# Kernel optimization log

Hardware: AMD Instinct MI355X
Metric: run time of the kernel (lower is better)

## Reference

```python
import jax, jax.numpy as jnp
import numpy as np

# Fixed supermask = [3, 4, 16, 28, 0, 0, 0, 3]:
#   preproc: relu(Linear x3); l1 = GCN(x); l2 = GCN(l1); l3 = GCN(l2);
#   out = relu(Linear z3((l1+l2+l3)/3))
HIDDEN = 64


def gcn_conv(h, W, b, src, dst, norm, n_nodes):
    # PyG GCNConv: h' = scatter_add(norm * (hW)[src] -> dst) + b
    hw = h @ W                                  # [N, F]
    msg = hw[src] * norm[:, None]               # gather + scale  [E+N, F]
    agg = jax.ops.segment_sum(msg, dst, num_segments=n_nodes)
    return agg + b


def setup_inputs() -> dict:
    key = jax.random.key(0)
    ks = jax.random.split(key, 12)
    N, E, NFEAT, NCLASS = 100000, 1000000, 256, 40
    x = jax.random.normal(ks[0], (N, NFEAT), dtype=jnp.float32)
    edge_index = jax.random.randint(ks[1], (2, E), 0, N, dtype=jnp.int64)
    s = 1.0 / np.sqrt(NFEAT)
    h = 1.0 / np.sqrt(HIDDEN)
    return {
        "x": x,
        "edge_index": edge_index,
        "Wx": jax.random.uniform(ks[2], (NFEAT, HIDDEN), jnp.float32, -s, s),
        "bx": jnp.zeros((HIDDEN,), jnp.float32),
        "W1": jax.random.uniform(ks[3], (HIDDEN, HIDDEN), jnp.float32, -h, h),
        "b1": jnp.zeros((HIDDEN,), jnp.float32),
        "W2": jax.random.uniform(ks[4], (HIDDEN, HIDDEN), jnp.float32, -h, h),
        "b2": jnp.zeros((HIDDEN,), jnp.float32),
        "W3": jax.random.uniform(ks[5], (HIDDEN, HIDDEN), jnp.float32, -h, h),
        "b3": jnp.zeros((HIDDEN,), jnp.float32),
        "Wz": jax.random.uniform(ks[6], (HIDDEN, NCLASS), jnp.float32, -h, h),
        "bz": jnp.zeros((NCLASS,), jnp.float32),
    }


def reference(x, edge_index, Wx, bx, W1, b1, W2, b2, W3, b3, Wz, bz):
    n = x.shape[0]
    # add self-loops (PyG GCNConv default)
    loop = jnp.arange(n, dtype=edge_index.dtype)
    src = jnp.concatenate([edge_index[0], loop])
    dst = jnp.concatenate([edge_index[1], loop])
    deg = jax.ops.segment_sum(jnp.ones_like(dst, dtype=x.dtype), dst, num_segments=n)
    dinv = jnp.where(deg > 0, jax.lax.rsqrt(deg), 0.0)
    norm = dinv[src] * dinv[dst]                 # [E+N]

    h0 = jax.nn.relu(x @ Wx + bx)                # x_3(relu) o x3(Linear)
    l1 = gcn_conv(h0, W1, b1, src, dst, norm, n)
    l2 = gcn_conv(l1, W2, b2, src, dst, norm, n)
    l3 = gcn_conv(l2, W3, b3, src, dst, norm, n)
    z = (l1 + l2 + l3) / 3.0
    return jax.nn.relu(z @ Wz + bz)
```

## Files before the change

### kernel.cpp

```cpp
#include <hip/hip_runtime.h>

#define NFEAT 256
#define HID 64
#define NCLASS 40
#define EPB 4096
#define BCAP 8192

typedef _Float16 half8 __attribute__((ext_vector_type(8)));
typedef float floatx4 __attribute__((ext_vector_type(4)));

__device__ __forceinline__ int wave_iscan(int v, int lane) {
    #pragma unroll
    for (int o = 1; o < 64; o <<= 1) {
        int u = __shfl_up(v, o, 64);
        if (lane >= o) v += u;
    }
    return v;
}

template<int NT>
__device__ __forceinline__ int block_iscan(int v, int t, int* wsum) {
    const int NW = NT / 64;
    int lane = t & 63, wv = t >> 6;
    int s = wave_iscan(v, lane);
    if (lane == 63) wsum[wv] = s;
    __syncthreads();
    if (wv == 0) {
        int w = (lane < NW) ? wsum[lane] : 0;
        int ws = wave_iscan(w, lane);
        if (lane < NW) wsum[lane] = ws;
    }
    __syncthreads();
    int add = (wv > 0) ? wsum[wv - 1] : 0;
    return s + add;
}

struct BinSM {
    int lcnt[256], loff[256], lcur[256], gbase[256], wsum[4];
    int sdst[EPB];
    int words[EPB];
};

__global__ __launch_bounds__(256) void k_pre(const int* __restrict__ src, const int* __restrict__ dst,
                                             int* __restrict__ bcur, int* __restrict__ bwords,
                                             int nbuckets, int E, int nbin,
                                             const float* __restrict__ W1, const float* __restrict__ W2,
                                             const float* __restrict__ W3, _Float16* __restrict__ Wt16) {
    __shared__ __align__(16) char smraw[sizeof(BinSM)];
    int t = threadIdx.x;
    int bid = blockIdx.x;

    if (bid >= nbin) {
        int l = bid - nbin;
        const float* Ws = (l == 0) ? W1 : (l == 1) ? W2 : W3;
        _Float16* wt = Wt16 + l * 4096;
        for (int i = t; i < 4096; i += 256) {
            int col = i >> 6, k = i & 63;
            wt[i] = (_Float16)Ws[k * HID + col];
        }
        return;
    }

    BinSM* sm = (BinSM*)smraw;
    int base = bid * EPB;
    int n = E - base; if (n > EPB) n = EPB;
    sm->lcnt[t] = 0;
    __syncthreads();
    for (int i = t; i < n; i += 256) {
        int d = dst[base + i];
        sm->sdst[i] = d;
        atomicAdd(&sm->lcnt[d >> 9], 1);
    }
    __syncthreads();
    int v = sm->lcnt[t];
    int incl = block_iscan<256>(v, t, sm->wsum);
    int excl = incl - v;
    sm->loff[t] = excl; sm->lcur[t] = excl;
    __syncthreads();
    for (int i = t; i < n; i += 256) {
        int d = sm->sdst[i], s = src[base + i];
        int b = d >> 9;
        int p = atomicAdd(&sm->lcur[b], 1);
        sm->words[p] = s | ((d & 511) << 17);
    }
    __syncthreads();
    if (t < nbuckets) {
        int c = sm->lcnt[t];
        sm->gbase[t] = c > 0 ? atomicAdd(&bcur[t], c) : 0;
    }
    __syncthreads();
    int lane = t & 63, wv = t >> 6;
    for (int b = wv; b < nbuckets; b += 4) {
        int o = sm->loff[b], c = sm->lcnt[b], gb = sm->gbase[b];
        int* dstp = bwords + (size_t)b * BCAP;
        for (int i = lane; i < c; i += 64) {
            int gp = gb + i;
            if (gp < BCAP) dstp[gp] = sm->words[o + i];
        }
    }
}

struct CsrSM {
    int cnt[512], cur[512], wsum[8];
    int lcsr[BCAP];
};

__global__ __launch_bounds__(512) void k_csr2(const int* __restrict__ bcur, const int* __restrict__ bwords,
                                              int* __restrict__ csr, unsigned* __restrict__ pk,
                                              float* __restrict__ dinv, int N, int ncsr,
                                              const float* __restrict__ x, const float* __restrict__ Wx,
                                              const float* __restrict__ bx, _Float16* __restrict__ h0,
                                              int ngemm) {
    __shared__ __align__(16) char smraw[sizeof(CsrSM)];
    int t = threadIdx.x;
    int bid = blockIdx.x;

    if (bid >= ncsr) {
        _Float16 (*Wt)[264] = (_Float16 (*)[264])smraw;
        {
            int c = t & 63, k0 = (t >> 6) * 32;
            for (int k = k0; k < k0 + 32; ++k)
                Wt[c][k] = (_Float16)Wx[k * HID + c];
        }
        __syncthreads();
        int lane = t & 63, lg = lane >> 4, ln = lane & 15;
        int wid = ((bid - ncsr) * 512 + t) >> 6;
        int nw = ngemm * 8;
        float bb[4];
        #pragma unroll
        for (int g = 0; g < 4; ++g) bb[g] = bx[g * 16 + ln];
        int ntiles = N >> 4;
        for (int tile = wid; tile < ntiles; tile += nw) {
            int row0 = tile << 4;
            const float* xr = x + (size_t)(row0 + ln) * NFEAT + lg * 8;
            float4 av[16];
            #pragma unroll
            for (int ks = 0; ks < 8; ++ks) {
                av[2 * ks]     = *(const float4*)(xr + ks * 32);
                av[2 * ks + 1] = *(const float4*)(xr + ks * 32 + 4);
            }
            floatx4 acc[4] = {{0.f,0.f,0.f,0.f},{0.f,0.f,0.f,0.f},{0.f,0.f,0.f,0.f},{0.f,0.f,0.f,0.f}};
            #pragma unroll
            for (int ks = 0; ks < 8; ++ks) {
                float4 a0 = av[2 * ks], a1 = av[2 * ks + 1];
                half8 a;
                a[0]=(_Float16)a0.x; a[1]=(_Float16)a0.y; a[2]=(_Float16)a0.z; a[3]=(_Float16)a0.w;
                a[4]=(_Float16)a1.x; a[5]=(_Float16)a1.y; a[6]=(_Float16)a1.z; a[7]=(_Float16)a1.w;
                #pragma unroll
                for (int g = 0; g < 4; ++g) {
                    half8 b = *(const half8*)&Wt[g * 16 + ln][ks * 32 + lg * 8];
                    acc[g] = __builtin_amdgcn_mfma_f32_16x16x32_f16(a, b, acc[g], 0, 0, 0);
                }
            }
            #pragma unroll
            for (int g = 0; g < 4; ++g) {
                #pragma unroll
                for (int r = 0; r < 4; ++r) {
                    int row = row0 + lg * 4 + r;
                    h0[(size_t)row * HID + g * 16 + ln] = (_Float16)fmaxf(acc[g][r] + bb[g], 0.f);
                }
            }
        }
        return;
    }

    CsrSM* sm = (CsrSM*)smraw;
    int b = bid;
    int nodebase = b << 9;
    int nb = bcur[b]; if (nb > BCAP) nb = BCAP;
    sm->cnt[t] = 0;
    __syncthreads();
    const int* wp = bwords + (size_t)b * BCAP;
    for (int i = t; i < nb; i += 512)
        atomicAdd(&sm->cnt[wp[i] >> 17], 1);
    __syncthreads();
    int v = sm->cnt[t];
    int incl = block_iscan<512>(v, t, sm->wsum);
    int excl = incl - v;
    sm->cur[t] = excl;
    int node = nodebase + t;
    if (node < N) {
        int c = v > 2047 ? 2047 : v;
        pk[node] = (unsigned)(b * BCAP + excl) | ((unsigned)c << 21);
        dinv[node] = rsqrtf((float)c + 1.0f);
    }
    __syncthreads();
    for (int i = t; i < nb; i += 512) {
        int w = wp[i];
        int pos = atomicAdd(&sm->cur[w >> 17], 1);
        sm->lcsr[pos] = w & 0x1FFFF;
    }
    __syncthreads();
    int* cp = csr + (size_t)b * BCAP;
    for (int i = t; i < nb; i += 512) cp[i] = sm->lcsr[i];
}

template<int WRN>
__global__ __launch_bounds__(256) void k_layer(const _Float16* __restrict__ Ph, const int* __restrict__ csr,
                                               const unsigned* __restrict__ pk, const float* __restrict__ dinv,
                                               const _Float16* __restrict__ Wt, const float* __restrict__ b,
                                               float* __restrict__ normf,
                                               _Float16* __restrict__ Lout, int N) {
    __shared__ _Float16 z[32][72];
    __shared__ _Float16 ot[32][72];
    int t = threadIdx.x;
    int lane = t & 63, wv = t >> 6;
    int sg = lane >> 3, f8 = lane & 7;
    int lg = lane >> 4, ln = lane & 15;
    int nb = blockIdx.x << 5;
    int node = nb + wv * 8 + sg;
    bool valid = node < N;
    int nodec = valid ? node : (N - 1);
    int col = wv * 16 + ln;
    half8 bf0 = *(const half8*)(Wt + col * 64 + lg * 8);
    half8 bf1 = *(const half8*)(Wt + col * 64 + 32 + lg * 8);
    float bb = b[col];

    unsigned pkv = valid ? pk[node] : 0u;
    int off = (int)(pkv & 0x1FFFFFu);
    int c = (int)(pkv >> 21);
    float dd = valid ? dinv[node] : 0.f;
    const _Float16* pb = Ph + f8 * 8;
    float acc[8];
    {
        half8 self = *(const half8*)(pb + (size_t)nodec * HID);
        float dd2 = dd * dd;
        #pragma unroll
        for (int j = 0; j < 8; ++j) acc[j] = (float)self[j] * dd2;
    }
    int ecur = f8;
    bool ok = ecur < c;
    int s_cur = ok ? csr[off + ecur] : nodec;
    float nm_cur;
    if (WRN) {
        nm_cur = ok ? dinv[s_cur] * dd : 0.f;
        if (ok) normf[off + ecur] = nm_cur;
    } else {
        nm_cur = ok ? normf[off + ecur] : 0.f;
    }
    for (int jj = 0; jj < c; jj += 8) {
        int en = jj + 8 + f8;
        bool okn = en < c;
        int s_nxt = okn ? csr[off + en] : nodec;
        float nm_nxt;
        if (WRN) {
            nm_nxt = okn ? dinv[s_nxt] * dd : 0.f;
            if (okn) normf[off + en] = nm_nxt;
        } else {
            nm_nxt = okn ? normf[off + en] : 0.f;
        }
        #pragma unroll
        for (int j = 0; j < 8; ++j) {
            int ss = __shfl(s_cur, j, 8);
            float nn = __shfl(nm_cur, j, 8);
            half8 v = *(const half8*)(pb + (size_t)ss * HID);
            #pragma unroll
            for (int q = 0; q < 8; ++q) acc[q] = fmaf((float)v[q], nn, acc[q]);
        }
        s_cur = s_nxt; nm_cur = nm_nxt;
    }
    {
        half8 zv;
        #pragma unroll
        for (int j = 0; j < 8; ++j) zv[j] = (_Float16)acc[j];
        *(half8*)&z[wv * 8 + sg][f8 * 8] = zv;
    }
    __syncthreads();
    floatx4 acc0 = {0.f, 0.f, 0.f, 0.f}, acc1 = {0.f, 0.f, 0.f, 0.f};
    {
        half8 a0 = *(const half8*)&z[ln][lg * 8];
        half8 a1 = *(const half8*)&z[16 + ln][lg * 8];
        acc0 = __builtin_amdgcn_mfma_f32_16x16x32_f16(a0, bf0, acc0, 0, 0, 0);
        acc1 = __builtin_amdgcn_mfma_f32_16x16x32_f16(a1, bf0, acc1, 0, 0, 0);
        a0 = *(const half8*)&z[ln][32 + lg * 8];
        a1 = *(const half8*)&z[16 + ln][32 + lg * 8];
        acc0 = __builtin_amdgcn_mfma_f32_16x16x32_f16(a0, bf1, acc0, 0, 0, 0);
        acc1 = __builtin_amdgcn_mfma_f32_16x16x32_f16(a1, bf1, acc1, 0, 0, 0);
    }
    #pragma unroll
    for (int r = 0; r < 4; ++r) {
        ot[lg * 4 + r][wv * 16 + ln] = (_Float16)(acc0[r] + bb);
        ot[16 + lg * 4 + r][wv * 16 + ln] = (_Float16)(acc1[r] + bb);
    }
    __syncthreads();
    {
        int row = t >> 3, c8 = t & 7;
        int onode = nb + row;
        if (onode < N)
            *(half8*)(Lout + (size_t)onode * HID + c8 * 8) = *(const half8*)&ot[row][c8 * 8];
    }
}

__global__ __launch_bounds__(256) void k_gemm_out(const _Float16* __restrict__ L1, const _Float16* __restrict__ L2,
                                                  const _Float16* __restrict__ L3, const float* __restrict__ Wz,
                                                  const float* __restrict__ bz, float* __restrict__ outp, int N) {
    int t = threadIdx.x;
    int lane = t & 63, lg = lane >> 4, ln = lane & 15;
    int wid = (blockIdx.x * 256 + t) >> 6;
    int nw = (gridDim.x * 256) >> 6;
    half8 b[2][3];
    float bb[3];
    #pragma unroll
    for (int g = 0; g < 3; ++g) {
        int col = g * 16 + ln;
        bb[g] = (col < NCLASS) ? bz[col] : 0.f;
        #pragma unroll
        for (int ks = 0; ks < 2; ++ks)
            #pragma unroll
            for (int j = 0; j < 8; ++j)
                b[ks][g][j] = (col < NCLASS) ? (_Float16)(Wz[(ks * 32 + lg * 8 + j) * NCLASS + col] * (1.f / 3.f)) : (_Float16)0.f;
    }
    int ntiles = N >> 4;
    for (int tile = wid; tile < ntiles; tile += nw) {
        int row0 = tile << 4;
        size_t rb = (size_t)(row0 + ln) * HID + lg * 8;
        floatx4 acc[3] = {{0.f,0.f,0.f,0.f},{0.f,0.f,0.f,0.f},{0.f,0.f,0.f,0.f}};
        #pragma unroll
        for (int ks = 0; ks < 2; ++ks) {
            half8 a1 = *(const half8*)(L1 + rb + ks * 32);
            half8 a2 = *(const half8*)(L2 + rb + ks * 32);
            half8 a3 = *(const half8*)(L3 + rb + ks * 32);
            half8 a;
            #pragma unroll
            for (int j = 0; j < 8; ++j)
                a[j] = (_Float16)((float)a1[j] + (float)a2[j] + (float)a3[j]);
            #pragma unroll
            for (int g = 0; g < 3; ++g)
                acc[g] = __builtin_amdgcn_mfma_f32_16x16x32_f16(a, b[ks][g], acc[g], 0, 0, 0);
        }
        #pragma unroll
        for (int g = 0; g < 3; ++g) {
            int col = g * 16 + ln;
            if (col < NCLASS) {
                #pragma unroll
                for (int r = 0; r < 4; ++r)
                    outp[(size_t)(row0 + lg * 4 + r) * NCLASS + col] = fmaxf(acc[g][r] + bb[g], 0.f);
            }
        }
    }
}

extern "C" void kernel_launch(void* const* d_in, const int* in_sizes, int n_in,
                              void* d_out, int out_size, void* d_ws, size_t ws_size,
                              hipStream_t stream) {
    const float* x  = (const float*)d_in[0];
    const int*   ei = (const int*)d_in[1];
    const float* Wx = (const float*)d_in[2];
    const float* bx = (const float*)d_in[3];
    const float* W1 = (const float*)d_in[4];
    const float* b1 = (const float*)d_in[5];
    const float* W2 = (const float*)d_in[6];
    const float* b2 = (const float*)d_in[7];
    const float* W3 = (const float*)d_in[8];
    const float* b3 = (const float*)d_in[9];
    const float* Wz = (const float*)d_in[10];
    const float* bz = (const float*)d_in[11];
    float* out = (float*)d_out;

    int N = in_sizes[0] / NFEAT;
    int E = in_sizes[1] / 2;
    const int* src = ei;
    const int* dst = ei + E;
    int nbuckets = (N + 511) >> 9;

    size_t nh = (size_t)N * HID;
    size_t Npad = ((size_t)N + 7) / 8 * 8;
    int*      bcur = (int*)d_ws;
    float*    dinv = (float*)d_ws + 256;
    unsigned* pk   = (unsigned*)(dinv + Npad);
    _Float16* H0   = (_Float16*)(pk + Npad);
    _Float16* L1   = H0 + nh;
    _Float16* L2   = L1 + nh;
    _Float16* L3   = L2 + nh;
    int*      bwords = (int*)(L3 + nh);
    int*      csr  = bwords + (size_t)nbuckets * BCAP;
    _Float16* Wt16 = (_Float16*)(csr + (size_t)nbuckets * BCAP);
    float*    normf = (float*)(Wt16 + 3 * 4096);

    int nbin = (E + EPB - 1) / EPB;
    int ngemm = 256;
    hipMemsetAsync(bcur, 0, 256 * sizeof(int), stream);
    k_pre<<<nbin + 3, 256, 0, stream>>>(src, dst, bcur, bwords, nbuckets, E, nbin, W1, W2, W3, Wt16);
    k_csr2<<<nbuckets + ngemm, 512, 0, stream>>>(bcur, bwords, csr, pk, dinv, N, nbuckets,
                                                 x, Wx, bx, H0, ngemm);

    int layer_blocks = (N + 31) / 32;
    k_layer<1><<<layer_blocks, 256, 0, stream>>>(H0, csr, pk, dinv, Wt16,          b1, normf, L1, N);
    k_layer<0><<<layer_blocks, 256, 0, stream>>>(L1, csr, pk, dinv, Wt16 + 4096,   b2, normf, L2, N);
    k_layer<0><<<layer_blocks, 256, 0, stream>>>(L2, csr, pk, dinv, Wt16 + 8192,   b3, normf, L3, N);

    k_gemm_out<<<512, 256, 0, stream>>>(L1, L2, L3, Wz, bz, out, N);
}
```

Before: 296.2 us.

## Build CSR via global degree atomics, per-bucket scan, and atomic fill

Replaces the two-pass shared-memory bucket sort (bin words into buckets, then locally sort each bucket) with three simpler kernels: global atomic degree counting, a per-512-node block scan that writes offsets and dinv, and an atomic-cursor fill that scatters source indices directly into CSR slots. This drops the intermediate bwords buffer and one full pass of edge traffic, and resizes the fused input GEMM to 256-thread blocks with more blocks. The cost is heavy global atomic contention on random destinations, and neighbor order within a row is now nondeterministic, which can change floating-point summation order.

```diff
diff --git a/kernel.cpp b/kernel.cpp
--- a/kernel.cpp
+++ b/kernel.cpp
@@ -3,7 +3,6 @@
 #define NFEAT 256
 #define HID 64
 #define NCLASS 40
-#define EPB 4096
 #define BCAP 8192
 
 typedef _Float16 half8 __attribute__((ext_vector_type(8)));
@@ -27,31 +26,26 @@
     __syncthreads();
     if (wv == 0) {
         int w = (lane < NW) ? wsum[lane] : 0;
-        int ws = wave_iscan(w, lane);
-        if (lane < NW) wsum[lane] = ws;
+        #pragma unroll
+        for (int o = 1; o < NW; o <<= 1) {
+            int u = __shfl_up(w, o, 64);
+            if (lane >= o) w += u;
+        }
+        if (lane < NW) wsum[lane] = w;
     }
     __syncthreads();
     int add = (wv > 0) ? wsum[wv - 1] : 0;
     return s + add;
 }
 
-struct BinSM {
-    int lcnt[256], loff[256], lcur[256], gbase[256], wsum[4];
-    int sdst[EPB];
-    int words[EPB];
-};
-
-__global__ __launch_bounds__(256) void k_pre(const int* __restrict__ src, const int* __restrict__ dst,
-                                             int* __restrict__ bcur, int* __restrict__ bwords,
-                                             int nbuckets, int E, int nbin,
+__global__ __launch_bounds__(256) void k_deg(const int* __restrict__ dst, int* __restrict__ deg,
+                                             int E, int ndeg,
                                              const float* __restrict__ W1, const float* __restrict__ W2,
                                              const float* __restrict__ W3, _Float16* __restrict__ Wt16) {
-    __shared__ __align__(16) char smraw[sizeof(BinSM)];
     int t = threadIdx.x;
     int bid = blockIdx.x;
-
-    if (bid >= nbin) {
-        int l = bid - nbin;
+    if (bid >= ndeg) {
+        int l = bid - ndeg;
         const float* Ws = (l == 0) ? W1 : (l == 1) ? W2 : W3;
         _Float16* wt = Wt16 + l * 4096;
         for (int i = t; i < 4096; i += 256) {
@@ -60,72 +54,50 @@
         }
         return;
     }
-
-    BinSM* sm = (BinSM*)smraw;
-    int base = bid * EPB;
-    int n = E - base; if (n > EPB) n = EPB;
-    sm->lcnt[t] = 0;
-    __syncthreads();
-    for (int i = t; i < n; i += 256) {
-        int d = dst[base + i];
-        sm->sdst[i] = d;
-        atomicAdd(&sm->lcnt[d >> 9], 1);
-    }
-    __syncthreads();
-    int v = sm->lcnt[t];
-    int incl = block_iscan<256>(v, t, sm->wsum);
+    int stride = ndeg * 256;
+    for (int i = bid * 256 + t; i < E; i += stride)
+        atomicAdd(&deg[dst[i]], 1);
+}
+
+__global__ __launch_bounds__(512) void k_off(const int* __restrict__ deg, unsigned* __restrict__ pk,
+                                             float* __restrict__ dinv, int N) {
+    __shared__ int wsum[8];
+    int t = threadIdx.x;
+    int b = blockIdx.x;
+    int node = (b << 9) + t;
+    int v = (node < N) ? deg[node] : 0;
+    int incl = block_iscan<512>(v, t, wsum);
     int excl = incl - v;
-    sm->loff[t] = excl; sm->lcur[t] = excl;
-    __syncthreads();
-    for (int i = t; i < n; i += 256) {
-        int d = sm->sdst[i], s = src[base + i];
-        int b = d >> 9;
-        int p = atomicAdd(&sm->lcur[b], 1);
-        sm->words[p] = s | ((d & 511) << 17);
-    }
-    __syncthreads();
-    if (t < nbuckets) {
-        int c = sm->lcnt[t];
-        sm->gbase[t] = c > 0 ? atomicAdd(&bcur[t], c) : 0;
-    }
-    __syncthreads();
-    int lane = t & 63, wv = t >> 6;
-    for (int b = wv; b < nbuckets; b += 4) {
-        int o = sm->loff[b], c = sm->lcnt[b], gb = sm->gbase[b];
-        int* dstp = bwords + (size_t)b * BCAP;
-        for (int i = lane; i < c; i += 64) {
-            int gp = gb + i;
-            if (gp < BCAP) dstp[gp] = sm->words[o + i];
-        }
-    }
-}
-
-struct CsrSM {
-    int cnt[512], cur[512], wsum[8];
-    int lcsr[BCAP];
-};
-
-__global__ __launch_bounds__(512) void k_csr2(const int* __restrict__ bcur, const int* __restrict__ bwords,
-                                              int* __restrict__ csr, unsigned* __restrict__ pk,
-                                              float* __restrict__ dinv, int N, int ncsr,
+    if (node < N) {
+        int c = v > 2047 ? 2047 : v;
+        if (excl >= BCAP) c = 0;
+        else if (excl + c > BCAP) c = BCAP - excl;
+        pk[node] = (unsigned)(b * BCAP + excl) | ((unsigned)c << 21);
+        dinv[node] = rsqrtf((float)c + 1.0f);
+    }
+}
+
+__global__ __launch_bounds__(256) void k_fill(const int* __restrict__ src, const int* __restrict__ dst,
+                                              const unsigned* __restrict__ pk, int* __restrict__ cnt,
+                                              int* __restrict__ csr, int E, int nfill,
                                               const float* __restrict__ x, const float* __restrict__ Wx,
                                               const float* __restrict__ bx, _Float16* __restrict__ h0,
-                                              int ngemm) {
-    __shared__ __align__(16) char smraw[sizeof(CsrSM)];
+                                              int N, int ngemm) {
+    __shared__ _Float16 Wt[64][264];
     int t = threadIdx.x;
     int bid = blockIdx.x;
 
-    if (bid >= ncsr) {
-        _Float16 (*Wt)[264] = (_Float16 (*)[264])smraw;
+    if (bid >= nfill) {
         {
-            int c = t & 63, k0 = (t >> 6) * 32;
-            for (int k = k0; k < k0 + 32; ++k)
+            int c = t & 63, k0 = (t >> 6) * 64;
+            for (int k = k0; k < k0 + 64; ++k)
                 Wt[c][k] = (_Float16)Wx[k * HID + c];
         }
         __syncthreads();
-        int lane = t & 63, lg = lane >> 4, ln = lane & 15;
-        int wid = ((bid - ncsr) * 512 + t) >> 6;
-        int nw = ngemm * 8;
+        int lane = t & 63, wv = t >> 6;
+        int lg = lane >> 4, ln = lane & 15;
+        int wid = (bid - nfill) * 4 + wv;
+        int nw = ngemm * 4;
         float bb[4];
         #pragma unroll
         for (int g = 0; g < 4; ++g) bb[g] = bx[g * 16 + ln];
@@ -164,35 +136,14 @@
         return;
     }
 
-    CsrSM* sm = (CsrSM*)smraw;
-    int b = bid;
-    int nodebase = b << 9;
-    int nb = bcur[b]; if (nb > BCAP) nb = BCAP;
-    sm->cnt[t] = 0;
-    __syncthreads();
-    const int* wp = bwords + (size_t)b * BCAP;
-    for (int i = t; i < nb; i += 512)
-        atomicAdd(&sm->cnt[wp[i] >> 17], 1);
-    __syncthreads();
-    int v = sm->cnt[t];
-    int incl = block_iscan<512>(v, t, sm->wsum);
-    int excl = incl - v;
-    sm->cur[t] = excl;
-    int node = nodebase + t;
-    if (node < N) {
-        int c = v > 2047 ? 2047 : v;
-        pk[node] = (unsigned)(b * BCAP + excl) | ((unsigned)c << 21);
-        dinv[node] = rsqrtf((float)c + 1.0f);
-    }
-    __syncthreads();
-    for (int i = t; i < nb; i += 512) {
-        int w = wp[i];
-        int pos = atomicAdd(&sm->cur[w >> 17], 1);
-        sm->lcsr[pos] = w & 0x1FFFF;
-    }
-    __syncthreads();
-    int* cp = csr + (size_t)b * BCAP;
-    for (int i = t; i < nb; i += 512) cp[i] = sm->lcsr[i];
+    int stride = nfill * 256;
+    for (int i = bid * 256 + t; i < E; i += stride) {
+        int d = dst[i], s = src[i];
+        unsigned p = pk[d];
+        int idx = atomicAdd(&cnt[d], 1);
+        if (idx < (int)(p >> 21))
+            csr[(p & 0x1FFFFFu) + idx] = s;
+    }
 }
 
 template<int WRN>
@@ -218,7 +169,7 @@
 
     unsigned pkv = valid ? pk[node] : 0u;
     int off = (int)(pkv & 0x1FFFFFu);
-    int c = (int)(pkv >> 21);
+    int c = valid ? (int)(pkv >> 21) : 0;
     float dd = valid ? dinv[node] : 0.f;
     const _Float16* pb = Ph + f8 * 8;
     float acc[8];
@@ -365,24 +316,24 @@
 
     size_t nh = (size_t)N * HID;
     size_t Npad = ((size_t)N + 7) / 8 * 8;
-    int*      bcur = (int*)d_ws;
-    float*    dinv = (float*)d_ws + 256;
+    int*      deg  = (int*)d_ws;
+    int*      cnt  = deg + Npad;
+    float*    dinv = (float*)(cnt + Npad);
     unsigned* pk   = (unsigned*)(dinv + Npad);
     _Float16* H0   = (_Float16*)(pk + Npad);
     _Float16* L1   = H0 + nh;
     _Float16* L2   = L1 + nh;
     _Float16* L3   = L2 + nh;
-    int*      bwords = (int*)(L3 + nh);
-    int*      csr  = bwords + (size_t)nbuckets * BCAP;
+    int*      csr  = (int*)(L3 + nh);
     _Float16* Wt16 = (_Float16*)(csr + (size_t)nbuckets * BCAP);
     float*    normf = (float*)(Wt16 + 3 * 4096);
 
-    int nbin = (E + EPB - 1) / EPB;
-    int ngemm = 256;
-    hipMemsetAsync(bcur, 0, 256 * sizeof(int), stream);
-    k_pre<<<nbin + 3, 256, 0, stream>>>(src, dst, bcur, bwords, nbuckets, E, nbin, W1, W2, W3, Wt16);
-    k_csr2<<<nbuckets + ngemm, 512, 0, stream>>>(bcur, bwords, csr, pk, dinv, N, nbuckets,
-                                                 x, Wx, bx, H0, ngemm);
+    int ndeg = 1024, nfill = 1024, ngemm = 512;
+    hipMemsetAsync(deg, 0, 2 * Npad * sizeof(int), stream);
+    k_deg<<<ndeg + 3, 256, 0, stream>>>(dst, deg, E, ndeg, W1, W2, W3, Wt16);
+    k_off<<<nbuckets, 512, 0, stream>>>(deg, pk, dinv, N);
+    k_fill<<<nfill + ngemm, 256, 0, stream>>>(src, dst, pk, cnt, csr, E, nfill,
+                                              x, Wx, bx, H0, N, ngemm);
 
     int layer_blocks = (N + 31) / 32;
     k_layer<1><<<layer_blocks, 256, 0, stream>>>(H0, csr, pk, dinv, Wt16,          b1, normf, L1, N);
```

Result: slower. 354.1 us (+19.5%).
